# Kernel tuning notes

Hardware: AMD Instinct MI355X
Metric: run time of the kernel (lower is better)

## Reference

```python
import jax, jax.numpy as jnp
import numpy as np
from jax import lax

NPOINT = 1024
NSAMPLE = 64
RADIUS = 0.2
EPS = 1e-5  # BatchNorm eps


def farthest_point_sample(xyz, npoint):
    # xyz: [B, N, 3] -> idx [B, npoint]; deterministic init at point 0
    B, N, _ = xyz.shape

    def step(carry, _):
        dist, farthest = carry
        centroid = jnp.take_along_axis(xyz, farthest[:, None, None], axis=1)  # [B,1,3]
        d = jnp.sum((xyz - centroid) ** 2, axis=-1)  # [B,N]
        dist = jnp.minimum(dist, d)
        new_far = jnp.argmax(dist, axis=-1).astype(jnp.int32)
        return (dist, new_far), farthest

    init = (jnp.full((B, N), 1e10, xyz.dtype), jnp.zeros((B,), jnp.int32))
    _, idxs = lax.scan(step, init, None, length=npoint)
    return jnp.transpose(idxs)  # [B, npoint]


def square_distance(src, dst):
    # src [B,S,3], dst [B,N,3] -> [B,S,N]
    d = -2.0 * jnp.einsum('bsc,bnc->bsn', src, dst)
    d += jnp.sum(src ** 2, -1)[:, :, None]
    d += jnp.sum(dst ** 2, -1)[:, None, :]
    return d


def query_ball_point(radius, nsample, xyz, new_xyz):
    B, N, _ = xyz.shape
    sqr = square_distance(new_xyz, xyz)  # [B,S,N]
    gi = jnp.where(sqr > radius ** 2, N, jnp.arange(N, dtype=jnp.int32))
    gi = jnp.sort(gi, axis=-1)[:, :, :nsample]  # [B,S,K]
    first = gi[:, :, :1]
    gi = jnp.where(gi == N, first, gi)
    return gi


def mlp_bn_relu(x, W, g, b):
    # x [B,S,K,Cin], W [Cin,Cout]; 1x1 conv + training-mode BN + ReLU
    y = jnp.einsum('bskc,co->bsko', x, W)
    m = jnp.mean(y, axis=(0, 1, 2))
    v = jnp.var(y, axis=(0, 1, 2))
    y = (y - m) * lax.rsqrt(v + EPS) * g + b
    return jax.nn.relu(y)


def setup_inputs() -> dict:
    key = jax.random.key(0)
    ks = jax.random.split(key, 8)
    B, N, C = 8, 4096, 128
    xyz = jax.random.uniform(ks[0], (B, N, 3), dtype=jnp.float32)
    features = jax.random.normal(ks[1], (B, C, N), dtype=jnp.float32)
    c_in = C + 3  # use_xyz
    W1 = jax.random.normal(ks[2], (c_in, 128), dtype=jnp.float32) * 0.05
    W2 = jax.random.normal(ks[3], (128, 128), dtype=jnp.float32) * 0.05
    W3 = jax.random.normal(ks[4], (128, 256), dtype=jnp.float32) * 0.05
    return {
        'xyz': xyz, 'features': features,
        'W1': W1, 'g1': jnp.ones((128,)), 'b1': jnp.zeros((128,)),
        'W2': W2, 'g2': jnp.ones((128,)), 'b2': jnp.zeros((128,)),
        'W3': W3, 'g3': jnp.ones((256,)), 'b3': jnp.zeros((256,)),
    }


def reference(xyz, features, W1, g1, b1, W2, g2, b2, W3, g3, b3):
    fps_idx = farthest_point_sample(xyz, NPOINT)              # [B,S]
    new_xyz = jnp.take_along_axis(xyz, fps_idx[:, :, None], axis=1)  # [B,S,3]
    gi = query_ball_point(RADIUS, NSAMPLE, xyz, new_xyz)      # [B,S,K]
    gather = jax.vmap(lambda p, i: p[i])                      # per-batch gather
    grouped_xyz = gather(xyz, gi) - new_xyz[:, :, None, :]    # [B,S,K,3]
    grouped_feat = gather(jnp.transpose(features, (0, 2, 1)), gi)  # [B,S,K,C]
    x = jnp.concatenate([grouped_xyz, grouped_feat], axis=-1)  # [B,S,K,3+C]
    x = mlp_bn_relu(x, W1, g1, b1)
    x = mlp_bn_relu(x, W2, g2, b2)
    x = mlp_bn_relu(x, W3, g3, b3)
    new_features = jnp.transpose(jnp.max(x, axis=2), (0, 2, 1))  # [B,256,S]
    return new_xyz, new_features
```

## Files before the change

### kernel.cpp

```cpp
#include <hip/hip_runtime.h>

#define B_  8
#define N_  4096
#define S_  1024
#define K_  64
#define CF_ 128
#define M_  (B_*S_*K_)

typedef __attribute__((ext_vector_type(8))) short bshort8;
typedef __attribute__((ext_vector_type(4))) float f32x4;
typedef __attribute__((ext_vector_type(4))) int   i32x4;
typedef __attribute__((ext_vector_type(2))) float f32x2;
typedef __attribute__((ext_vector_type(4))) unsigned short us4;

__device__ __forceinline__ unsigned short f2bf(float f){
  unsigned int u = __float_as_uint(f);
  u = u + 0x7FFFu + ((u >> 16) & 1u);
  return (unsigned short)(u >> 16);
}
__device__ __forceinline__ float bf2f(unsigned short h){
  return __uint_as_float(((unsigned int)h) << 16);
}

#define DPP_PAIR_STEP(CTRL)                                                     \
  {                                                                             \
    int _vi = __builtin_amdgcn_update_dpp(__float_as_int(best), __float_as_int(best), (CTRL), 0xF, 0xF, false); \
    int _ii = __builtin_amdgcn_update_dpp(bidx, bidx, (CTRL), 0xF, 0xF, false); \
    float _ov = __int_as_float(_vi);                                            \
    bool _tk = (_ov > best) || (_ov == best && _ii < bidx);                     \
    best = _tk ? _ov : best;                                                    \
    bidx = _tk ? _ii : bidx;                                                    \
  }

__global__ __launch_bounds__(256) void fps_kernel(const float* __restrict__ xyz,
                                                  float* __restrict__ nx_out,
                                                  float* __restrict__ nx_ws){
#pragma clang fp contract(off)
  __shared__ float sx[N_], sy[N_], sz[N_];
  __shared__ int   sidx[S_];
  __shared__ alignas(16) float redv[2][4];
  __shared__ alignas(16) int   redi[2][4];
  const int b = blockIdx.x, t = threadIdx.x;
  const int lane = t & 63, w = t >> 6;
  const float* xb = xyz + (size_t)b*N_*3;
  f32x2 px[8], py[8], pz[8], dist[8];
#pragma unroll
  for (int j=0;j<8;++j){
    int i0 = (2*j)*256 + t, i1 = (2*j+1)*256 + t;
    float x0=xb[i0*3+0], y0=xb[i0*3+1], z0=xb[i0*3+2];
    float x1=xb[i1*3+0], y1=xb[i1*3+1], z1=xb[i1*3+2];
    px[j] = (f32x2){x0,x1}; py[j] = (f32x2){y0,y1}; pz[j] = (f32x2){z0,z1};
    dist[j] = (f32x2){1e10f,1e10f};
    sx[i0]=x0; sy[i0]=y0; sz[i0]=z0;
    sx[i1]=x1; sy[i1]=y1; sz[i1]=z1;
  }
  __syncthreads();
  int farthest = 0;
  for (int it=0; it<S_; ++it){
    if (t==0) sidx[it] = farthest;
    float cx = sx[farthest], cy = sy[farthest], cz = sz[farthest];
    f32x2 cx2 = (f32x2){cx,cx}, cy2 = (f32x2){cy,cy}, cz2 = (f32x2){cz,cz};
    float best = -1.0f; int bidx = 0;
#pragma unroll
    for (int j=0;j<8;++j){
      f32x2 dx = px[j] - cx2;
      f32x2 dy = py[j] - cy2;
      f32x2 dz = pz[j] - cz2;
      f32x2 d  = (dx*dx + dy*dy) + dz*dz;
      f32x2 nd;
      nd.x = fminf(dist[j].x, d.x);
      nd.y = fminf(dist[j].y, d.y);
      dist[j] = nd;
      bool tk0 = nd.x > best;
      best = tk0 ? nd.x : best;
      bidx = tk0 ? ((2*j)*256 + t) : bidx;
      bool tk1 = nd.y > best;
      best = tk1 ? nd.y : best;
      bidx = tk1 ? ((2*j+1)*256 + t) : bidx;
    }
    DPP_PAIR_STEP(0xB1);
    DPP_PAIR_STEP(0x4E);
    DPP_PAIR_STEP(0x124);
    DPP_PAIR_STEP(0x128);
    DPP_PAIR_STEP(0x142);
    DPP_PAIR_STEP(0x143);
    const int buf = it & 1;
    if (lane == 63){ redv[buf][w] = best; redi[buf][w] = bidx; }
    __syncthreads();
    f32x4 vv = *(const f32x4*)&redv[buf][0];
    i32x4 iv = *(const i32x4*)&redi[buf][0];
    float v01 = vv[0]; int i01 = iv[0];
    { bool tk = (vv[1] > v01) || (vv[1] == v01 && iv[1] < i01); v01 = tk?vv[1]:v01; i01 = tk?iv[1]:i01; }
    float v23 = vv[2]; int i23 = iv[2];
    { bool tk = (vv[3] > v23) || (vv[3] == v23 && iv[3] < i23); v23 = tk?vv[3]:v23; i23 = tk?iv[3]:i23; }
    { bool tk = (v23 > v01) || (v23 == v01 && i23 < i01); v01 = tk?v23:v01; i01 = tk?i23:i01; }
    farthest = i01;
  }
  __syncthreads();
  for (int i=t; i<S_; i+=256){
    int id = sidx[i];
    size_t base = (size_t)(b*S_+i)*3;
    float vx=sx[id], vy=sy[id], vz=sz[id];
    nx_out[base+0]=vx; nx_out[base+1]=vy; nx_out[base+2]=vz;
    nx_ws[base+0]=vx;  nx_ws[base+1]=vy;  nx_ws[base+2]=vz;
  }
}

__global__ __launch_bounds__(256) void qbp_kernel(const float* __restrict__ xyz,
                                                  const float* __restrict__ nx,
                                                  int* __restrict__ gi){
  const double R2 = 0.2*0.2;
  int gtid = blockIdx.x*256 + threadIdx.x;
  int wid = gtid >> 6, lane = gtid & 63;
  int b = wid >> 10, s = wid & 1023;
  const float* xb = xyz + (size_t)b*N_*3;
  const float* c  = nx + (size_t)(b*S_+s)*3;
  double cx=(double)c[0], cy=(double)c[1], cz=(double)c[2];
  double cc = cx*cx + cy*cy + cz*cz;
  int* g = gi + (size_t)(b*S_+s)*K_;
  int count = 0, first = -1;
  for (int ch=0; ch<64 && count<K_; ++ch){
    int i = ch*64 + lane;
    double x = (double)xb[i*3+0], y = (double)xb[i*3+1], z = (double)xb[i*3+2];
    double e  = cx*x + cy*y + cz*z;
    double pp = x*x + y*y + z*z;
    double d  = -2.0*e + cc + pp;
    bool keep = !(d > R2);
    unsigned long long bal = __ballot(keep);
    int pos = count + __builtin_popcountll(bal & ((1ull<<lane)-1ull));
    if (keep && pos < K_) g[pos] = i;
    if (first < 0 && bal) first = ch*64 + (int)__builtin_ctzll(bal);
    count += __builtin_popcountll(bal);
  }
  if (count < K_){
    int p = count + lane;
    if (p < K_) g[p] = first;
  }
}

__global__ __launch_bounds__(256) void transpose_kernel(const float* __restrict__ f,
                                                        unsigned short* __restrict__ ft){
  __shared__ float tile[32][33];
  int b = blockIdx.z, ct = blockIdx.y, nt = blockIdx.x;
  int tx = threadIdx.x & 31, ty = threadIdx.x >> 5;
#pragma unroll
  for (int r=0; r<32; r+=8)
    tile[ty+r][tx] = f[((size_t)(b*128 + ct*32 + ty + r))*4096 + nt*32 + tx];
  __syncthreads();
#pragma unroll
  for (int r=0; r<32; r+=8){
    int n = nt*32 + ty + r, cc = ct*32 + tx;
    ft[((size_t)b*4096 + n)*128 + cc] = f2bf(tile[tx][ty+r]);
  }
}

__global__ void wprep_kernel(const float* __restrict__ W1, const float* __restrict__ W2,
                             const float* __restrict__ W3,
                             unsigned short* __restrict__ Wt1, unsigned short* __restrict__ Wt2,
                             unsigned short* __restrict__ Wt3){
  int t = blockIdx.x*blockDim.x + threadIdx.x;
  int stride = gridDim.x*blockDim.x;
  for (int idx=t; idx<128*160; idx+=stride){
    int n = idx/160, k = idx-(idx/160)*160;
    float v = 0.f;
    if (k < 128) v = W1[(k+3)*128 + n];
    else if (k < 131) v = W1[(k-128)*128 + n];
    Wt1[idx] = f2bf(v);
  }
  for (int idx=t; idx<128*128; idx+=stride){
    int n = idx>>7, k = idx&127;
    Wt2[idx] = f2bf(W2[k*128+n]);
  }
  for (int idx=t; idx<256*128; idx+=stride){
    int n = idx>>7, k = idx&127;
    Wt3[idx] = f2bf(W3[k*256+n]);
  }
}

__global__ __launch_bounds__(256,2) void pgemm_kernel(const unsigned short* __restrict__ featT,
                                                      const unsigned short* __restrict__ Wt1,
                                                      float* __restrict__ P){
  __shared__ alignas(16) unsigned short At[128*40];
  __shared__ alignas(16) unsigned short Bt[128*40];
  const int t = threadIdx.x, blk = blockIdx.x;
  const size_t rowBase = (size_t)blk*128;
  const int lane = t&63, wave = t>>6;
  const int wm = wave>>1, wn = wave&1;
  const int lrow = lane&15, quad = lane>>4;
  f32x4 acc[4][4];
  const f32x4 z4 = {0.f,0.f,0.f,0.f};
#pragma unroll
  for (int i=0;i<4;++i)
#pragma unroll
    for (int j=0;j<4;++j) acc[i][j]=z4;
  for (int ch=0; ch<4; ++ch){
    __syncthreads();
#pragma unroll
    for (int half=0; half<2; ++half){
      int sl = t + half*256; int r = sl>>2, p = sl&3;
      *(bshort8*)&At[r*40+p*8] = *(const bshort8*)(featT + (rowBase + r)*CF_ + ch*32 + p*8);
      *(bshort8*)&Bt[r*40+p*8] = *(const bshort8*)(Wt1 + r*160 + ch*32 + p*8);
    }
    __syncthreads();
    bshort8 af[4], bfr[4];
#pragma unroll
    for (int mt=0; mt<4; ++mt) af[mt]  = *(const bshort8*)&At[(wm*64+mt*16+lrow)*40 + quad*8];
#pragma unroll
    for (int nt=0; nt<4; ++nt) bfr[nt] = *(const bshort8*)&Bt[(wn*64+nt*16+lrow)*40 + quad*8];
#pragma unroll
    for (int mt=0; mt<4; ++mt)
#pragma unroll
      for (int nt=0; nt<4; ++nt)
        acc[mt][nt] = __builtin_amdgcn_mfma_f32_16x16x32_bf16(af[mt], bfr[nt], acc[mt][nt], 0,0,0);
  }
#pragma unroll
  for (int mt=0; mt<4; ++mt)
#pragma unroll
    for (int nt=0; nt<4; ++nt)
#pragma unroll
      for (int r=0; r<4; ++r){
        int row = wm*64 + mt*16 + quad*4 + r;
        int col = wn*64 + nt*16 + lrow;
        P[(rowBase + row)*128 + col] = acc[mt][nt][r];
      }
}

template<int PHASE>
__global__ __launch_bounds__(256,2) void mm_fused(
    const float* __restrict__ P,
    const float* __restrict__ W1,
    const unsigned short* __restrict__ Wt2,
    const unsigned short* __restrict__ Wt3,
    const int* __restrict__ gi,
    const float* __restrict__ xyz,
    const float* __restrict__ nxyz,
    const float* __restrict__ ss1,
    const float* __restrict__ ss2,
    float* __restrict__ slots,
    float* __restrict__ minv,
    float* __restrict__ maxv)
{
  __shared__ alignas(16) unsigned short Bt[2][(PHASE>=2)?(128*40):8];
  __shared__ alignas(16) unsigned short Y[(PHASE>=2)?(128*136):16];
  __shared__ int giL[128];
  __shared__ alignas(16) float dxL[128][4];
  __shared__ alignas(16) float w0L[128], w1L[128], w2L[128];
  __shared__ float sLDS[(PHASE==1)?128:4], s2LDS[(PHASE==1)?128:4];

  const int t = threadIdx.x;
  const int mblk = blockIdx.x;
  const int b = mblk >> 9;
  const int lane = t&63, wave = t>>6;
  const int wm = wave>>1, wn = wave&1;
  const int lrow = lane&15, quad = lane>>4;
  const int slot = mblk & 63;

  if (t<128){
    int i = gi[(size_t)mblk*128 + t];
    giL[t] = i;
    int s = ((mblk*128 + t) >> 6) & 1023;
    const float* pp = xyz  + ((size_t)b*N_ + i)*3;
    const float* qq = nxyz + (size_t)(b*S_ + s)*3;
    dxL[t][0] = __fsub_rn(pp[0],qq[0]);
    dxL[t][1] = __fsub_rn(pp[1],qq[1]);
    dxL[t][2] = __fsub_rn(pp[2],qq[2]);
    w0L[t] = W1[t]; w1L[t] = W1[128+t]; w2L[t] = W1[256+t];
    if constexpr (PHASE==1){ sLDS[t]=0.f; s2LDS[t]=0.f; }
  }
  __syncthreads();

  {
    const int rgrp = t>>5, cq = (t&31)*4;
    f32x4 w0 = *(const f32x4*)&w0L[cq];
    f32x4 w1 = *(const f32x4*)&w1L[cq];
    f32x4 w2 = *(const f32x4*)&w2L[cq];
    f32x4 a1v, b1v;
    if constexpr (PHASE>=2){
      a1v = *(const f32x4*)(ss1 + cq);
      b1v = *(const f32x4*)(ss1 + 128 + cq);
    }
    f32x4 sA = {0,0,0,0}, s2A = {0,0,0,0};
#pragma unroll
    for (int g=0; g<16; ++g){
      int r = g*8 + rgrp;
      int pi = giL[r];
      f32x4 p = *(const f32x4*)(P + ((size_t)b*N_ + pi)*128 + cq);
      float dx = dxL[r][0], dy = dxL[r][1], dz = dxL[r][2];
      f32x4 y;
#pragma unroll
      for (int e=0;e<4;++e)
        y[e] = fmaf(dz, w2[e], fmaf(dy, w1[e], fmaf(dx, w0[e], p[e])));
      if constexpr (PHASE==1){
#pragma unroll
        for (int e=0;e<4;++e){ sA[e] += y[e]; s2A[e] = fmaf(y[e], y[e], s2A[e]); }
      } else {
        us4 zz;
#pragma unroll
        for (int e=0;e<4;++e)
          zz[e] = f2bf(fmaxf(fmaf(y[e], a1v[e], b1v[e]), 0.f));
        *(us4*)&Y[r*136 + cq] = zz;
      }
    }
    if constexpr (PHASE==1){
#pragma unroll
      for (int e=0;e<4;++e){
        atomicAdd(&sLDS[cq+e],  sA[e]);
        atomicAdd(&s2LDS[cq+e], s2A[e]);
      }
      __syncthreads();
      if (t<128){
        atomicAdd(&slots[(slot*128+t)*2+0], sLDS[t]);
        atomicAdd(&slots[(slot*128+t)*2+1], s2LDS[t]);
      }
      return;
    }
  }

  if constexpr (PHASE>=2){
    f32x4 acc[4][4];
    const f32x4 z4 = {0.f,0.f,0.f,0.f};
#pragma unroll
    for (int i=0;i<4;++i)
#pragma unroll
      for (int j=0;j<4;++j) acc[i][j]=z4;

    {
      bshort8 bV[2];
#pragma unroll
      for (int half=0; half<2; ++half){
        int sl = t + half*256; int r = sl>>2, p = sl&3;
        bV[half] = *(const bshort8*)(Wt2 + r*128 + p*8);
      }
#pragma unroll
      for (int half=0; half<2; ++half){
        int sl = t + half*256; int r = sl>>2, p = sl&3;
        *(bshort8*)&Bt[1][r*40+p*8] = bV[half];
      }
      for (int ch=0; ch<4; ++ch){
        const int cur = (ch & 1) ^ 1;
        __syncthreads();
        bshort8 af[4], bfr[4];
#pragma unroll
        for (int mt=0; mt<4; ++mt) af[mt]  = *(const bshort8*)&Y[(wm*64+mt*16+lrow)*136 + ch*32 + quad*8];
#pragma unroll
        for (int nt=0; nt<4; ++nt) bfr[nt] = *(const bshort8*)&Bt[cur][(wn*64+nt*16+lrow)*40 + quad*8];
        if (ch < 3){
#pragma unroll
          for (int half=0; half<2; ++half){
            int sl = t + half*256; int r = sl>>2, p = sl&3;
            bV[half] = *(const bshort8*)(Wt2 + r*128 + (ch+1)*32 + p*8);
          }
        }
#pragma unroll
        for (int mt=0; mt<4; ++mt)
#pragma unroll
          for (int nt=0; nt<4; ++nt)
            acc[mt][nt] = __builtin_amdgcn_mfma_f32_16x16x32_bf16(af[mt], bfr[nt], acc[mt][nt], 0,0,0);
        if (ch < 3){
          const int nxt = cur ^ 1;
#pragma unroll
          for (int half=0; half<2; ++half){
            int sl = t + half*256; int r = sl>>2, p = sl&3;
            *(bshort8*)&Bt[nxt][r*40+p*8] = bV[half];
          }
        }
      }
    }

    if constexpr (PHASE==2){
#pragma unroll
      for (int nt=0; nt<4; ++nt){
        float s=0.f, s2=0.f;
#pragma unroll
        for (int mt=0; mt<4; ++mt)
#pragma unroll
          for (int r=0; r<4; ++r){ float v=acc[mt][nt][r]; s+=v; s2=fmaf(v,v,s2); }
        s  += __shfl_xor(s,16,64);  s  += __shfl_xor(s,32,64);
        s2 += __shfl_xor(s2,16,64); s2 += __shfl_xor(s2,32,64);
        if (lane<16){
          int c = wn*64+nt*16+lane;
          atomicAdd(&slots[(slot*128+c)*2+0], s);
          atomicAdd(&slots[(slot*128+c)*2+1], s2);
        }
      }
      return;
    }

    if constexpr (PHASE==3){
      __syncthreads();
#pragma unroll
      for (int nt=0; nt<4; ++nt){
        int c = wn*64+nt*16+lrow;
        float sc = ss2[c], sh = ss2[128+c];
#pragma unroll
        for (int mt=0; mt<4; ++mt)
#pragma unroll
          for (int r=0; r<4; ++r){
            int row = wm*64+mt*16+quad*4+r;
            Y[row*136 + c] = f2bf(fmaxf(fmaf(acc[mt][nt][r], sc, sh), 0.f));
          }
      }

      for (int h=0; h<2; ++h){
#pragma unroll
        for (int i=0;i<4;++i)
#pragma unroll
          for (int j=0;j<4;++j) acc[i][j]=z4;
        bshort8 bV[2];
#pragma unroll
        for (int half=0; half<2; ++half){
          int sl = t + half*256; int r = sl>>2, p = sl&3;
          bV[half] = *(const bshort8*)(Wt3 + ((size_t)(h*128+r))*128 + p*8);
        }
#pragma unroll
        for (int half=0; half<2; ++half){
          int sl = t + half*256; int r = sl>>2, p = sl&3;
          *(bshort8*)&Bt[1][r*40+p*8] = bV[half];
        }
        for (int ch=0; ch<4; ++ch){
          const int cur = (ch & 1) ^ 1;
          __syncthreads();
          bshort8 af[4], bfr[4];
#pragma unroll
          for (int mt=0; mt<4; ++mt) af[mt]  = *(const bshort8*)&Y[(wm*64+mt*16+lrow)*136 + ch*32 + quad*8];
#pragma unroll
          for (int nt=0; nt<4; ++nt) bfr[nt] = *(const bshort8*)&Bt[cur][(wn*64+nt*16+lrow)*40 + quad*8];
          if (ch < 3){
#pragma unroll
            for (int half=0; half<2; ++half){
              int sl = t + half*256; int r = sl>>2, p = sl&3;
              bV[half] = *(const bshort8*)(Wt3 + ((size_t)(h*128+r))*128 + (ch+1)*32 + p*8);
            }
          }
#pragma unroll
          for (int mt=0; mt<4; ++mt)
#pragma unroll
            for (int nt=0; nt<4; ++nt)
              acc[mt][nt] = __builtin_amdgcn_mfma_f32_16x16x32_bf16(af[mt], bfr[nt], acc[mt][nt], 0,0,0);
          if (ch < 3){
            const int nxt = cur ^ 1;
#pragma unroll
            for (int half=0; half<2; ++half){
              int sl = t + half*256; int r = sl>>2, p = sl&3;
              *(bshort8*)&Bt[nxt][r*40+p*8] = bV[half];
            }
          }
        }
#pragma unroll
        for (int nt=0; nt<4; ++nt){
          float s=0.f, s2=0.f, mx=-3.0e38f, mn=3.0e38f;
#pragma unroll
          for (int mt=0; mt<4; ++mt)
#pragma unroll
            for (int r=0; r<4; ++r){
              float v=acc[mt][nt][r];
              s+=v; s2=fmaf(v,v,s2);
              mx=fmaxf(mx,v); mn=fminf(mn,v);
            }
          s  += __shfl_xor(s,16,64);  s  += __shfl_xor(s,32,64);
          s2 += __shfl_xor(s2,16,64); s2 += __shfl_xor(s2,32,64);
          mx = fmaxf(mx, __shfl_xor(mx,16,64)); mx = fmaxf(mx, __shfl_xor(mx,32,64));
          mn = fminf(mn, __shfl_xor(mn,16,64)); mn = fminf(mn, __shfl_xor(mn,32,64));
          if (lane<16){
            int c = h*128 + wn*64+nt*16+lane;
            atomicAdd(&slots[(slot*256+c)*2+0], s);
            atomicAdd(&slots[(slot*256+c)*2+1], s2);
            size_t sidx = (size_t)mblk*2 + wm;
            maxv[sidx*256 + c] = mx;
            minv[sidx*256 + c] = mn;
          }
        }
      }
    }
  }
}

__global__ void stats_kernel(const float* __restrict__ slots, const float* __restrict__ g,
                             const float* __restrict__ beta, float* __restrict__ ssOut,
                             int C, float inv_cnt){
  int c = threadIdx.x;
  if (c >= C) return;
  float s=0.f, s2=0.f;
  for (int k=0;k<64;++k){
    s  += slots[(k*C + c)*2 + 0];
    s2 += slots[(k*C + c)*2 + 1];
  }
  float m = s * inv_cnt;
  float v = fmaxf(s2 * inv_cnt - m*m, 0.f);
  float sc = rsqrtf(v + 1e-5f) * g[c];
  ssOut[c] = sc;
  ssOut[C + c] = beta[c] - m*sc;
}

__global__ __launch_bounds__(256) void final_kernel(const float* __restrict__ minv,
                                                    const float* __restrict__ maxv,
                                                    const float* __restrict__ ss3,
                                                    float* __restrict__ out){
  __shared__ float tile[64][65];
  const int t = threadIdx.x;
  const int cb = blockIdx.x;
  const int sb = blockIdx.y;
  const int b  = blockIdx.z;
  const int w = t>>6, l = t&63;
  {
    int c = cb*64 + l;
    float sc = ss3[c], sh = ss3[256+c];
#pragma unroll
    for (int k=0;k<16;++k){
      int sl = k*4 + w;
      size_t mi = ((size_t)(b*1024 + sb*64 + sl))*256 + c;
      float v = (sc >= 0.f) ? maxv[mi] : minv[mi];
      tile[sl][l] = fmaxf(fmaf(v, sc, sh), 0.f);
    }
  }
  __syncthreads();
#pragma unroll
  for (int k=0;k<16;++k){
    int cl = k*4 + w;
    out[((size_t)(b*256 + cb*64 + cl))*1024 + sb*64 + l] = tile[l][cl];
  }
}

extern "C" void kernel_launch(void* const* d_in, const int* in_sizes, int n_in,
                              void* d_out, int out_size, void* d_ws, size_t ws_size,
                              hipStream_t stream){
  const float* xyz      = (const float*)d_in[0];
  const float* features = (const float*)d_in[1];
  const float* W1 = (const float*)d_in[2];
  const float* g1 = (const float*)d_in[3];
  const float* b1 = (const float*)d_in[4];
  const float* W2 = (const float*)d_in[5];
  const float* g2 = (const float*)d_in[6];
  const float* b2 = (const float*)d_in[7];
  const float* W3 = (const float*)d_in[8];
  const float* g3 = (const float*)d_in[9];
  const float* b3 = (const float*)d_in[10];
  float* out = (float*)d_out;

  char* ws = (char*)d_ws;
  size_t off = 0;
  auto alloc = [&](size_t bytes)->char*{
    char* p = ws + off;
    off = (off + bytes + 255) & ~(size_t)255;
    return p;
  };
  float* slots1 = (float*)alloc((size_t)64*128*2*4);
  float* slots2 = (float*)alloc((size_t)64*128*2*4);
  float* slots3 = (float*)alloc((size_t)64*256*2*4);
  float* ss1    = (float*)alloc(256*4);
  float* ss2    = (float*)alloc(256*4);
  float* ss3    = (float*)alloc(512*4);
  float* nxyz   = (float*)alloc((size_t)24576*4);
  int*   gi     = (int*)  alloc((size_t)M_*4);
  unsigned short* featT = (unsigned short*)alloc((size_t)B_*N_*CF_*2);
  unsigned short* Wt1   = (unsigned short*)alloc((size_t)128*160*2);
  unsigned short* Wt2   = (unsigned short*)alloc((size_t)128*128*2);
  unsigned short* Wt3   = (unsigned short*)alloc((size_t)256*128*2);
  float* minv = (float*)alloc((size_t)B_*S_*256*4);
  float* maxv = (float*)alloc((size_t)B_*S_*256*4);
  float* P    = (float*)alloc((size_t)B_*N_*128*4);

  hipMemsetAsync(slots1, 0, (size_t)(64*128*2 + 64*128*2 + 64*256*2)*4, stream);

  transpose_kernel<<<dim3(128,4,8), 256, 0, stream>>>(features, featT);
  wprep_kernel<<<64, 256, 0, stream>>>(W1, W2, W3, Wt1, Wt2, Wt3);
  pgemm_kernel<<<256, 256, 0, stream>>>(featT, Wt1, P);
  fps_kernel<<<8, 256, 0, stream>>>(xyz, out, nxyz);
  qbp_kernel<<<2048, 256, 0, stream>>>(xyz, nxyz, gi);

  const float inv_cnt = 1.0f / (float)M_;
  mm_fused<1><<<4096, 256, 0, stream>>>(P, W1, Wt2, Wt3, gi, xyz, nxyz,
                                        nullptr, nullptr, slots1, nullptr, nullptr);
  stats_kernel<<<1, 128, 0, stream>>>(slots1, g1, b1, ss1, 128, inv_cnt);
  mm_fused<2><<<4096, 256, 0, stream>>>(P, W1, Wt2, Wt3, gi, xyz, nxyz,
                                        ss1, nullptr, slots2, nullptr, nullptr);
  stats_kernel<<<1, 128, 0, stream>>>(slots2, g2, b2, ss2, 128, inv_cnt);
  mm_fused<3><<<4096, 256, 0, stream>>>(P, W1, Wt2, Wt3, gi, xyz, nxyz,
                                        ss1, ss2, slots3, minv, maxv);
  stats_kernel<<<1, 256, 0, stream>>>(slots3, g3, b3, ss3, 256, inv_cnt);
  final_kernel<<<dim3(4,16,8), 256, 0, stream>>>(minv, maxv, ss3, out + 24576);
}
```

Measured before the change: 1.144 ms.

## Merge prep kernels, co-schedule FPS with feature GEMM, fuse ball query with layer-1 stats

The transpose and weight-prep kernels are merged into one launch. The serial 8-block FPS kernel now shares a launch with the 256-block feature GEMM, so the GEMM blocks run on otherwise idle CUs while FPS iterates. The ball query is fused with the layer-1 statistics pass, which removes the separate mm_fused<1> launch and the re-read of gi. The tradeoffs are a larger shared-memory footprint for the combined kernel and one wave per centroid doing the stats loop.

```diff
diff --git a/kernel.cpp b/kernel.cpp
--- a/kernel.cpp
+++ b/kernel.cpp
@@ -20,6 +20,49 @@
 }
 __device__ __forceinline__ float bf2f(unsigned short h){
   return __uint_as_float(((unsigned int)h) << 16);
+}
+
+__global__ __launch_bounds__(256) void prep_kernel(const float* __restrict__ f,
+                                                   const float* __restrict__ W1,
+                                                   const float* __restrict__ W2,
+                                                   const float* __restrict__ W3,
+                                                   unsigned short* __restrict__ ft,
+                                                   unsigned short* __restrict__ Wt1,
+                                                   unsigned short* __restrict__ Wt2,
+                                                   unsigned short* __restrict__ Wt3){
+  __shared__ float tile[32][33];
+  const int blk = blockIdx.x;
+  if (blk < 4096){
+    int nt = blk & 127, ct = (blk>>7)&3, b = blk>>9;
+    int tx = threadIdx.x & 31, ty = threadIdx.x >> 5;
+#pragma unroll
+    for (int r=0; r<32; r+=8)
+      tile[ty+r][tx] = f[((size_t)(b*128 + ct*32 + ty + r))*4096 + nt*32 + tx];
+    __syncthreads();
+#pragma unroll
+    for (int r=0; r<32; r+=8){
+      int n = nt*32 + ty + r, cc = ct*32 + tx;
+      ft[((size_t)b*4096 + n)*128 + cc] = f2bf(tile[tx][ty+r]);
+    }
+  } else {
+    int t = (blk-4096)*256 + threadIdx.x;
+    int stride = 64*256;
+    for (int idx=t; idx<128*160; idx+=stride){
+      int n = idx/160, k = idx-(idx/160)*160;
+      float v = 0.f;
+      if (k < 128) v = W1[(k+3)*128 + n];
+      else if (k < 131) v = W1[(k-128)*128 + n];
+      Wt1[idx] = f2bf(v);
+    }
+    for (int idx=t; idx<128*128; idx+=stride){
+      int n = idx>>7, k = idx&127;
+      Wt2[idx] = f2bf(W2[k*128+n]);
+    }
+    for (int idx=t; idx<256*128; idx+=stride){
+      int n = idx>>7, k = idx&127;
+      Wt3[idx] = f2bf(W3[k*256+n]);
+    }
+  }
 }
 
 #define DPP_PAIR_STEP(CTRL)                                                     \
@@ -32,197 +75,207 @@
     bidx = _tk ? _ii : bidx;                                                    \
   }
 
-__global__ __launch_bounds__(256) void fps_kernel(const float* __restrict__ xyz,
-                                                  float* __restrict__ nx_out,
-                                                  float* __restrict__ nx_ws){
+__global__ __launch_bounds__(256) void fps_pgemm_kernel(const float* __restrict__ xyz,
+                                                        float* __restrict__ nx_out,
+                                                        float* __restrict__ nx_ws,
+                                                        const unsigned short* __restrict__ featT,
+                                                        const unsigned short* __restrict__ Wt1,
+                                                        float* __restrict__ P){
 #pragma clang fp contract(off)
-  __shared__ float sx[N_], sy[N_], sz[N_];
-  __shared__ int   sidx[S_];
-  __shared__ alignas(16) float redv[2][4];
-  __shared__ alignas(16) int   redi[2][4];
-  const int b = blockIdx.x, t = threadIdx.x;
+  __shared__ alignas(16) char smem[53312];
+  const int t = threadIdx.x;
+  if (blockIdx.x < 8){
+    float* sx = (float*)smem;
+    float* sy = (float*)(smem+16384);
+    float* sz = (float*)(smem+32768);
+    int*   sidx = (int*)(smem+49152);
+    float (*redv)[4] = (float(*)[4])(smem+53248);
+    int   (*redi)[4] = (int(*)[4])(smem+53280);
+    const int b = blockIdx.x;
+    const int lane = t & 63, w = t >> 6;
+    const float* xb = xyz + (size_t)b*N_*3;
+    f32x2 px[8], py[8], pz[8], dist[8];
+#pragma unroll
+    for (int j=0;j<8;++j){
+      int i0 = (2*j)*256 + t, i1 = (2*j+1)*256 + t;
+      float x0=xb[i0*3+0], y0=xb[i0*3+1], z0=xb[i0*3+2];
+      float x1=xb[i1*3+0], y1=xb[i1*3+1], z1=xb[i1*3+2];
+      px[j] = (f32x2){x0,x1}; py[j] = (f32x2){y0,y1}; pz[j] = (f32x2){z0,z1};
+      dist[j] = (f32x2){1e10f,1e10f};
+      sx[i0]=x0; sy[i0]=y0; sz[i0]=z0;
+      sx[i1]=x1; sy[i1]=y1; sz[i1]=z1;
+    }
+    __syncthreads();
+    int farthest = 0;
+    for (int it=0; it<S_; ++it){
+      if (t==0) sidx[it] = farthest;
+      float cx = sx[farthest], cy = sy[farthest], cz = sz[farthest];
+      f32x2 cx2 = (f32x2){cx,cx}, cy2 = (f32x2){cy,cy}, cz2 = (f32x2){cz,cz};
+      float best = -1.0f; int bidx = 0;
+#pragma unroll
+      for (int j=0;j<8;++j){
+        f32x2 dx = px[j] - cx2;
+        f32x2 dy = py[j] - cy2;
+        f32x2 dz = pz[j] - cz2;
+        f32x2 d  = (dx*dx + dy*dy) + dz*dz;
+        f32x2 nd;
+        nd.x = fminf(dist[j].x, d.x);
+        nd.y = fminf(dist[j].y, d.y);
+        dist[j] = nd;
+        bool tk0 = nd.x > best;
+        best = tk0 ? nd.x : best;
+        bidx = tk0 ? ((2*j)*256 + t) : bidx;
+        bool tk1 = nd.y > best;
+        best = tk1 ? nd.y : best;
+        bidx = tk1 ? ((2*j+1)*256 + t) : bidx;
+      }
+      DPP_PAIR_STEP(0xB1);
+      DPP_PAIR_STEP(0x4E);
+      DPP_PAIR_STEP(0x124);
+      DPP_PAIR_STEP(0x128);
+      DPP_PAIR_STEP(0x142);
+      DPP_PAIR_STEP(0x143);
+      const int buf = it & 1;
+      if (lane == 63){ redv[buf][w] = best; redi[buf][w] = bidx; }
+      __syncthreads();
+      f32x4 vv = *(const f32x4*)&redv[buf][0];
+      i32x4 iv = *(const i32x4*)&redi[buf][0];
+      float v01 = vv[0]; int i01 = iv[0];
+      { bool tk = (vv[1] > v01) || (vv[1] == v01 && iv[1] < i01); v01 = tk?vv[1]:v01; i01 = tk?iv[1]:i01; }
+      float v23 = vv[2]; int i23 = iv[2];
+      { bool tk = (vv[3] > v23) || (vv[3] == v23 && iv[3] < i23); v23 = tk?vv[3]:v23; i23 = tk?iv[3]:i23; }
+      { bool tk = (v23 > v01) || (v23 == v01 && i23 < i01); v01 = tk?v23:v01; i01 = tk?i23:i01; }
+      farthest = i01;
+    }
+    __syncthreads();
+    for (int i=t; i<S_; i+=256){
+      int id = sidx[i];
+      size_t base = (size_t)(b*S_+i)*3;
+      float vx=sx[id], vy=sy[id], vz=sz[id];
+      nx_out[base+0]=vx; nx_out[base+1]=vy; nx_out[base+2]=vz;
+      nx_ws[base+0]=vx;  nx_ws[base+1]=vy;  nx_ws[base+2]=vz;
+    }
+  } else {
+    unsigned short* At = (unsigned short*)smem;
+    unsigned short* Bt = (unsigned short*)(smem+10240);
+    const int blk = blockIdx.x - 8;
+    const size_t rowBase = (size_t)blk*128;
+    const int lane = t&63, wave = t>>6;
+    const int wm = wave>>1, wn = wave&1;
+    const int lrow = lane&15, quad = lane>>4;
+    f32x4 acc[4][4];
+    const f32x4 z4 = {0.f,0.f,0.f,0.f};
+#pragma unroll
+    for (int i=0;i<4;++i)
+#pragma unroll
+      for (int j=0;j<4;++j) acc[i][j]=z4;
+    for (int ch=0; ch<4; ++ch){
+      __syncthreads();
+#pragma unroll
+      for (int half=0; half<2; ++half){
+        int sl = t + half*256; int r = sl>>2, p = sl&3;
+        *(bshort8*)&At[r*40+p*8] = *(const bshort8*)(featT + (rowBase + r)*CF_ + ch*32 + p*8);
+        *(bshort8*)&Bt[r*40+p*8] = *(const bshort8*)(Wt1 + r*160 + ch*32 + p*8);
+      }
+      __syncthreads();
+      bshort8 af[4], bfr[4];
+#pragma unroll
+      for (int mt=0; mt<4; ++mt) af[mt]  = *(const bshort8*)&At[(wm*64+mt*16+lrow)*40 + quad*8];
+#pragma unroll
+      for (int nt=0; nt<4; ++nt) bfr[nt] = *(const bshort8*)&Bt[(wn*64+nt*16+lrow)*40 + quad*8];
+#pragma unroll
+      for (int mt=0; mt<4; ++mt)
+#pragma unroll
+        for (int nt=0; nt<4; ++nt)
+          acc[mt][nt] = __builtin_amdgcn_mfma_f32_16x16x32_bf16(af[mt], bfr[nt], acc[mt][nt], 0,0,0);
+    }
+#pragma unroll
+    for (int mt=0; mt<4; ++mt)
+#pragma unroll
+      for (int nt=0; nt<4; ++nt)
+#pragma unroll
+        for (int r=0; r<4; ++r){
+          int row = wm*64 + mt*16 + quad*4 + r;
+          int col = wn*64 + nt*16 + lrow;
+          P[(rowBase + row)*128 + col] = acc[mt][nt][r];
+        }
+  }
+}
+
+__global__ __launch_bounds__(256) void qbp_y1_kernel(const float* __restrict__ xyz,
+                                                     const float* __restrict__ nx,
+                                                     const float* __restrict__ P,
+                                                     const float* __restrict__ W1,
+                                                     int* __restrict__ gi,
+                                                     float* __restrict__ slots){
+  __shared__ int giW[4][64];
+  __shared__ alignas(16) float dxL[4][64][4];
+  __shared__ float sLDS[128], s2LDS[128];
+  const int t = threadIdx.x;
   const int lane = t & 63, w = t >> 6;
+  if (t < 128){ sLDS[t]=0.f; s2LDS[t]=0.f; }
+  __syncthreads();
+  const int wid = blockIdx.x*4 + w;
+  const int b = wid >> 10, s = wid & 1023;
   const float* xb = xyz + (size_t)b*N_*3;
-  f32x2 px[8], py[8], pz[8], dist[8];
-#pragma unroll
-  for (int j=0;j<8;++j){
-    int i0 = (2*j)*256 + t, i1 = (2*j+1)*256 + t;
-    float x0=xb[i0*3+0], y0=xb[i0*3+1], z0=xb[i0*3+2];
-    float x1=xb[i1*3+0], y1=xb[i1*3+1], z1=xb[i1*3+2];
-    px[j] = (f32x2){x0,x1}; py[j] = (f32x2){y0,y1}; pz[j] = (f32x2){z0,z1};
-    dist[j] = (f32x2){1e10f,1e10f};
-    sx[i0]=x0; sy[i0]=y0; sz[i0]=z0;
-    sx[i1]=x1; sy[i1]=y1; sz[i1]=z1;
+  {
+    const double R2 = 0.2*0.2;
+    const float* c  = nx + (size_t)(b*S_+s)*3;
+    double cx=(double)c[0], cy=(double)c[1], cz=(double)c[2];
+    double cc = cx*cx + cy*cy + cz*cz;
+    int* g = gi + (size_t)(b*S_+s)*K_;
+    int count = 0, first = -1;
+    for (int ch=0; ch<64 && count<K_; ++ch){
+      int i = ch*64 + lane;
+      double x = (double)xb[i*3+0], y = (double)xb[i*3+1], z = (double)xb[i*3+2];
+      double e  = cx*x + cy*y + cz*z;
+      double pp = x*x + y*y + z*z;
+      double d  = -2.0*e + cc + pp;
+      bool keep = !(d > R2);
+      unsigned long long bal = __ballot(keep);
+      int pos = count + __builtin_popcountll(bal & ((1ull<<lane)-1ull));
+      if (keep && pos < K_){ g[pos] = i; giW[w][pos] = i; }
+      if (first < 0 && bal) first = ch*64 + (int)__builtin_ctzll(bal);
+      count += __builtin_popcountll(bal);
+    }
+    if (count < K_){
+      int p = count + lane;
+      if (p < K_){ g[p] = first; giW[w][p] = first; }
+    }
+    int i = giW[w][lane];
+    const float* pp = xyz + ((size_t)b*N_ + i)*3;
+    const float* qq = nx  + (size_t)(b*S_ + s)*3;
+    dxL[w][lane][0] = __fsub_rn(pp[0],qq[0]);
+    dxL[w][lane][1] = __fsub_rn(pp[1],qq[1]);
+    dxL[w][lane][2] = __fsub_rn(pp[2],qq[2]);
+  }
+  {
+    const int cq = lane*2;
+    f32x2 w0 = *(const f32x2*)(W1 + cq);
+    f32x2 w1v = *(const f32x2*)(W1 + 128 + cq);
+    f32x2 w2 = *(const f32x2*)(W1 + 256 + cq);
+    f32x2 sA = {0,0}, s2A = {0,0};
+#pragma unroll 4
+    for (int r=0; r<64; ++r){
+      int pi = giW[w][r];
+      f32x2 p = *(const f32x2*)(P + ((size_t)b*N_ + pi)*128 + cq);
+      float dx = dxL[w][r][0], dy = dxL[w][r][1], dz = dxL[w][r][2];
+      f32x2 y;
+#pragma unroll
+      for (int e=0;e<2;++e)
+        y[e] = fmaf(dz, w2[e], fmaf(dy, w1v[e], fmaf(dx, w0[e], p[e])));
+      sA.x += y.x; sA.y += y.y;
+      s2A.x = fmaf(y.x,y.x,s2A.x); s2A.y = fmaf(y.y,y.y,s2A.y);
+    }
+    atomicAdd(&sLDS[cq],    sA.x);  atomicAdd(&sLDS[cq+1],  sA.y);
+    atomicAdd(&s2LDS[cq],   s2A.x); atomicAdd(&s2LDS[cq+1], s2A.y);
   }
   __syncthreads();
-  int farthest = 0;
-  for (int it=0; it<S_; ++it){
-    if (t==0) sidx[it] = farthest;
-    float cx = sx[farthest], cy = sy[farthest], cz = sz[farthest];
-    f32x2 cx2 = (f32x2){cx,cx}, cy2 = (f32x2){cy,cy}, cz2 = (f32x2){cz,cz};
-    float best = -1.0f; int bidx = 0;
-#pragma unroll
-    for (int j=0;j<8;++j){
-      f32x2 dx = px[j] - cx2;
-      f32x2 dy = py[j] - cy2;
-      f32x2 dz = pz[j] - cz2;
-      f32x2 d  = (dx*dx + dy*dy) + dz*dz;
-      f32x2 nd;
-      nd.x = fminf(dist[j].x, d.x);
-      nd.y = fminf(dist[j].y, d.y);
-      dist[j] = nd;
-      bool tk0 = nd.x > best;
-      best = tk0 ? nd.x : best;
-      bidx = tk0 ? ((2*j)*256 + t) : bidx;
-      bool tk1 = nd.y > best;
-      best = tk1 ? nd.y : best;
-      bidx = tk1 ? ((2*j+1)*256 + t) : bidx;
-    }
-    DPP_PAIR_STEP(0xB1);
-    DPP_PAIR_STEP(0x4E);
-    DPP_PAIR_STEP(0x124);
-    DPP_PAIR_STEP(0x128);
-    DPP_PAIR_STEP(0x142);
-    DPP_PAIR_STEP(0x143);
-    const int buf = it & 1;
-    if (lane == 63){ redv[buf][w] = best; redi[buf][w] = bidx; }
-    __syncthreads();
-    f32x4 vv = *(const f32x4*)&redv[buf][0];
-    i32x4 iv = *(const i32x4*)&redi[buf][0];
-    float v01 = vv[0]; int i01 = iv[0];
-    { bool tk = (vv[1] > v01) || (vv[1] == v01 && iv[1] < i01); v01 = tk?vv[1]:v01; i01 = tk?iv[1]:i01; }
-    float v23 = vv[2]; int i23 = iv[2];
-    { bool tk = (vv[3] > v23) || (vv[3] == v23 && iv[3] < i23); v23 = tk?vv[3]:v23; i23 = tk?iv[3]:i23; }
-    { bool tk = (v23 > v01) || (v23 == v01 && i23 < i01); v01 = tk?v23:v01; i01 = tk?i23:i01; }
-    farthest = i01;
-  }
-  __syncthreads();
-  for (int i=t; i<S_; i+=256){
-    int id = sidx[i];
-    size_t base = (size_t)(b*S_+i)*3;
-    float vx=sx[id], vy=sy[id], vz=sz[id];
-    nx_out[base+0]=vx; nx_out[base+1]=vy; nx_out[base+2]=vz;
-    nx_ws[base+0]=vx;  nx_ws[base+1]=vy;  nx_ws[base+2]=vz;
-  }
-}
-
-__global__ __launch_bounds__(256) void qbp_kernel(const float* __restrict__ xyz,
-                                                  const float* __restrict__ nx,
-                                                  int* __restrict__ gi){
-  const double R2 = 0.2*0.2;
-  int gtid = blockIdx.x*256 + threadIdx.x;
-  int wid = gtid >> 6, lane = gtid & 63;
-  int b = wid >> 10, s = wid & 1023;
-  const float* xb = xyz + (size_t)b*N_*3;
-  const float* c  = nx + (size_t)(b*S_+s)*3;
-  double cx=(double)c[0], cy=(double)c[1], cz=(double)c[2];
-  double cc = cx*cx + cy*cy + cz*cz;
-  int* g = gi + (size_t)(b*S_+s)*K_;
-  int count = 0, first = -1;
-  for (int ch=0; ch<64 && count<K_; ++ch){
-    int i = ch*64 + lane;
-    double x = (double)xb[i*3+0], y = (double)xb[i*3+1], z = (double)xb[i*3+2];
-    double e  = cx*x + cy*y + cz*z;
-    double pp = x*x + y*y + z*z;
-    double d  = -2.0*e + cc + pp;
-    bool keep = !(d > R2);
-    unsigned long long bal = __ballot(keep);
-    int pos = count + __builtin_popcountll(bal & ((1ull<<lane)-1ull));
-    if (keep && pos < K_) g[pos] = i;
-    if (first < 0 && bal) first = ch*64 + (int)__builtin_ctzll(bal);
-    count += __builtin_popcountll(bal);
-  }
-  if (count < K_){
-    int p = count + lane;
-    if (p < K_) g[p] = first;
-  }
-}
-
-__global__ __launch_bounds__(256) void transpose_kernel(const float* __restrict__ f,
-                                                        unsigned short* __restrict__ ft){
-  __shared__ float tile[32][33];
-  int b = blockIdx.z, ct = blockIdx.y, nt = blockIdx.x;
-  int tx = threadIdx.x & 31, ty = threadIdx.x >> 5;
-#pragma unroll
-  for (int r=0; r<32; r+=8)
-    tile[ty+r][tx] = f[((size_t)(b*128 + ct*32 + ty + r))*4096 + nt*32 + tx];
-  __syncthreads();
-#pragma unroll
-  for (int r=0; r<32; r+=8){
-    int n = nt*32 + ty + r, cc = ct*32 + tx;
-    ft[((size_t)b*4096 + n)*128 + cc] = f2bf(tile[tx][ty+r]);
-  }
-}
-
-__global__ void wprep_kernel(const float* __restrict__ W1, const float* __restrict__ W2,
-                             const float* __restrict__ W3,
-                             unsigned short* __restrict__ Wt1, unsigned short* __restrict__ Wt2,
-                             unsigned short* __restrict__ Wt3){
-  int t = blockIdx.x*blockDim.x + threadIdx.x;
-  int stride = gridDim.x*blockDim.x;
-  for (int idx=t; idx<128*160; idx+=stride){
-    int n = idx/160, k = idx-(idx/160)*160;
-    float v = 0.f;
-    if (k < 128) v = W1[(k+3)*128 + n];
-    else if (k < 131) v = W1[(k-128)*128 + n];
-    Wt1[idx] = f2bf(v);
-  }
-  for (int idx=t; idx<128*128; idx+=stride){
-    int n = idx>>7, k = idx&127;
-    Wt2[idx] = f2bf(W2[k*128+n]);
-  }
-  for (int idx=t; idx<256*128; idx+=stride){
-    int n = idx>>7, k = idx&127;
-    Wt3[idx] = f2bf(W3[k*256+n]);
-  }
-}
-
-__global__ __launch_bounds__(256,2) void pgemm_kernel(const unsigned short* __restrict__ featT,
-                                                      const unsigned short* __restrict__ Wt1,
-                                                      float* __restrict__ P){
-  __shared__ alignas(16) unsigned short At[128*40];
-  __shared__ alignas(16) unsigned short Bt[128*40];
-  const int t = threadIdx.x, blk = blockIdx.x;
-  const size_t rowBase = (size_t)blk*128;
-  const int lane = t&63, wave = t>>6;
-  const int wm = wave>>1, wn = wave&1;
-  const int lrow = lane&15, quad = lane>>4;
-  f32x4 acc[4][4];
-  const f32x4 z4 = {0.f,0.f,0.f,0.f};
-#pragma unroll
-  for (int i=0;i<4;++i)
-#pragma unroll
-    for (int j=0;j<4;++j) acc[i][j]=z4;
-  for (int ch=0; ch<4; ++ch){
-    __syncthreads();
-#pragma unroll
-    for (int half=0; half<2; ++half){
-      int sl = t + half*256; int r = sl>>2, p = sl&3;
-      *(bshort8*)&At[r*40+p*8] = *(const bshort8*)(featT + (rowBase + r)*CF_ + ch*32 + p*8);
-      *(bshort8*)&Bt[r*40+p*8] = *(const bshort8*)(Wt1 + r*160 + ch*32 + p*8);
-    }
-    __syncthreads();
-    bshort8 af[4], bfr[4];
-#pragma unroll
-    for (int mt=0; mt<4; ++mt) af[mt]  = *(const bshort8*)&At[(wm*64+mt*16+lrow)*40 + quad*8];
-#pragma unroll
-    for (int nt=0; nt<4; ++nt) bfr[nt] = *(const bshort8*)&Bt[(wn*64+nt*16+lrow)*40 + quad*8];
-#pragma unroll
-    for (int mt=0; mt<4; ++mt)
-#pragma unroll
-      for (int nt=0; nt<4; ++nt)
-        acc[mt][nt] = __builtin_amdgcn_mfma_f32_16x16x32_bf16(af[mt], bfr[nt], acc[mt][nt], 0,0,0);
-  }
-#pragma unroll
-  for (int mt=0; mt<4; ++mt)
-#pragma unroll
-    for (int nt=0; nt<4; ++nt)
-#pragma unroll
-      for (int r=0; r<4; ++r){
-        int row = wm*64 + mt*16 + quad*4 + r;
-        int col = wn*64 + nt*16 + lrow;
-        P[(rowBase + row)*128 + col] = acc[mt][nt][r];
-      }
+  if (t < 128){
+    int slot = blockIdx.x & 63;
+    atomicAdd(&slots[(slot*128+t)*2+0], sLDS[t]);
+    atomicAdd(&slots[(slot*128+t)*2+1], s2LDS[t]);
+  }
 }
 
 template<int PHASE>
@@ -240,12 +293,11 @@
     float* __restrict__ minv,
     float* __restrict__ maxv)
 {
-  __shared__ alignas(16) unsigned short Bt[2][(PHASE>=2)?(128*40):8];
-  __shared__ alignas(16) unsigned short Y[(PHASE>=2)?(128*136):16];
+  __shared__ alignas(16) unsigned short Bt[2][128*40];
+  __shared__ alignas(16) unsigned short Y[128*136];
   __shared__ int giL[128];
   __shared__ alignas(16) float dxL[128][4];
   __shared__ alignas(16) float w0L[128], w1L[128], w2L[128];
-  __shared__ float sLDS[(PHASE==1)?128:4], s2LDS[(PHASE==1)?128:4];
 
   const int t = threadIdx.x;
   const int mblk = blockIdx.x;
@@ -265,7 +317,6 @@
     dxL[t][1] = __fsub_rn(pp[1],qq[1]);
     dxL[t][2] = __fsub_rn(pp[2],qq[2]);
     w0L[t] = W1[t]; w1L[t] = W1[128+t]; w2L[t] = W1[256+t];
-    if constexpr (PHASE==1){ sLDS[t]=0.f; s2LDS[t]=0.f; }
   }
   __syncthreads();
 
@@ -274,12 +325,8 @@
     f32x4 w0 = *(const f32x4*)&w0L[cq];
     f32x4 w1 = *(const f32x4*)&w1L[cq];
     f32x4 w2 = *(const f32x4*)&w2L[cq];
-    f32x4 a1v, b1v;
-    if constexpr (PHASE>=2){
-      a1v = *(const f32x4*)(ss1 + cq);
-      b1v = *(const f32x4*)(ss1 + 128 + cq);
-    }
-    f32x4 sA = {0,0,0,0}, s2A = {0,0,0,0};
+    f32x4 a1v = *(const f32x4*)(ss1 + cq);
+    f32x4 b1v = *(const f32x4*)(ss1 + 128 + cq);
 #pragma unroll
     for (int g=0; g<16; ++g){
       int r = g*8 + rgrp;
@@ -290,46 +337,108 @@
 #pragma unroll
       for (int e=0;e<4;++e)
         y[e] = fmaf(dz, w2[e], fmaf(dy, w1[e], fmaf(dx, w0[e], p[e])));
-      if constexpr (PHASE==1){
-#pragma unroll
-        for (int e=0;e<4;++e){ sA[e] += y[e]; s2A[e] = fmaf(y[e], y[e], s2A[e]); }
-      } else {
-        us4 zz;
-#pragma unroll
-        for (int e=0;e<4;++e)
-          zz[e] = f2bf(fmaxf(fmaf(y[e], a1v[e], b1v[e]), 0.f));
-        *(us4*)&Y[r*136 + cq] = zz;
-      }
-    }
-    if constexpr (PHASE==1){
-#pragma unroll
-      for (int e=0;e<4;++e){
-        atomicAdd(&sLDS[cq+e],  sA[e]);
-        atomicAdd(&s2LDS[cq+e], s2A[e]);
-      }
+      us4 zz;
+#pragma unroll
+      for (int e=0;e<4;++e)
+        zz[e] = f2bf(fmaxf(fmaf(y[e], a1v[e], b1v[e]), 0.f));
+      *(us4*)&Y[r*136 + cq] = zz;
+    }
+  }
+
+  f32x4 acc[4][4];
+  const f32x4 z4 = {0.f,0.f,0.f,0.f};
+#pragma unroll
+  for (int i=0;i<4;++i)
+#pragma unroll
+    for (int j=0;j<4;++j) acc[i][j]=z4;
+
+  {
+    bshort8 bV[2];
+#pragma unroll
+    for (int half=0; half<2; ++half){
+      int sl = t + half*256; int r = sl>>2, p = sl&3;
+      bV[half] = *(const bshort8*)(Wt2 + r*128 + p*8);
+    }
+#pragma unroll
+    for (int half=0; half<2; ++half){
+      int sl = t + half*256; int r = sl>>2, p = sl&3;
+      *(bshort8*)&Bt[1][r*40+p*8] = bV[half];
+    }
+    for (int ch=0; ch<4; ++ch){
+      const int cur = (ch & 1) ^ 1;
       __syncthreads();
-      if (t<128){
-        atomicAdd(&slots[(slot*128+t)*2+0], sLDS[t]);
-        atomicAdd(&slots[(slot*128+t)*2+1], s2LDS[t]);
-      }
-      return;
-    }
-  }
-
-  if constexpr (PHASE>=2){
-    f32x4 acc[4][4];
-    const f32x4 z4 = {0.f,0.f,0.f,0.f};
-#pragma unroll
-    for (int i=0;i<4;++i)
-#pragma unroll
-      for (int j=0;j<4;++j) acc[i][j]=z4;
-
-    {
+      bshort8 af[4], bfr[4];
+#pragma unroll
+      for (int mt=0; mt<4; ++mt) af[mt]  = *(const bshort8*)&Y[(wm*64+mt*16+lrow)*136 + ch*32 + quad*8];
+#pragma unroll
+      for (int nt=0; nt<4; ++nt) bfr[nt] = *(const bshort8*)&Bt[cur][(wn*64+nt*16+lrow)*40 + quad*8];
+      if (ch < 3){
+#pragma unroll
+        for (int half=0; half<2; ++half){
+          int sl = t + half*256; int r = sl>>2, p = sl&3;
+          bV[half] = *(const bshort8*)(Wt2 + r*128 + (ch+1)*32 + p*8);
+        }
+      }
+#pragma unroll
+      for (int mt=0; mt<4; ++mt)
+#pragma unroll
+        for (int nt=0; nt<4; ++nt)
+          acc[mt][nt] = __builtin_amdgcn_mfma_f32_16x16x32_bf16(af[mt], bfr[nt], acc[mt][nt], 0,0,0);
+      if (ch < 3){
+        const int nxt = cur ^ 1;
+#pragma unroll
+        for (int half=0; half<2; ++half){
+          int sl = t + half*256; int r = sl>>2, p = sl&3;
+          *(bshort8*)&Bt[nxt][r*40+p*8] = bV[half];
+        }
+      }
+    }
+  }
+
+  if constexpr (PHASE==2){
+#pragma unroll
+    for (int nt=0; nt<4; ++nt){
+      float s=0.f, s2=0.f;
+#pragma unroll
+      for (int mt=0; mt<4; ++mt)
+#pragma unroll
+        for (int r=0; r<4; ++r){ float v=acc[mt][nt][r]; s+=v; s2=fmaf(v,v,s2); }
+      s  += __shfl_xor(s,16,64);  s  += __shfl_xor(s,32,64);
+      s2 += __shfl_xor(s2,16,64); s2 += __shfl_xor(s2,32,64);
+      if (lane<16){
+        int c = wn*64+nt*16+lane;
+        atomicAdd(&slots[(slot*128+c)*2+0], s);
+        atomicAdd(&slots[(slot*128+c)*2+1], s2);
+      }
+    }
+    return;
+  }
+
+  if constexpr (PHASE==3){
+    __syncthreads();
+#pragma unroll
+    for (int nt=0; nt<4; ++nt){
+      int c = wn*64+nt*16+lrow;
+      float sc = ss2[c], sh = ss2[128+c];
+#pragma unroll
+      for (int mt=0; mt<4; ++mt)
+#pragma unroll
+        for (int r=0; r<4; ++r){
+          int row = wm*64+mt*16+quad*4+r;
+          Y[row*136 + c] = f2bf(fmaxf(fmaf(acc[mt][nt][r], sc, sh), 0.f));
+        }
+    }
+
+    for (int h=0; h<2; ++h){
+#pragma unroll
+      for (int i=0;i<4;++i)
+#pragma unroll
+        for (int j=0;j<4;++j) acc[i][j]=z4;
       bshort8 bV[2];
 #pragma unroll
       for (int half=0; half<2; ++half){
         int sl = t + half*256; int r = sl>>2, p = sl&3;
-        bV[half] = *(const bshort8*)(Wt2 + r*128 + p*8);
+        bV[half] = *(const bshort8*)(Wt3 + ((size_t)(h*128+r))*128 + p*8);
       }
 #pragma unroll
       for (int half=0; half<2; ++half){
@@ -348,7 +457,7 @@
 #pragma unroll
           for (int half=0; half<2; ++half){
             int sl = t + half*256; int r = sl>>2, p = sl&3;
-            bV[half] = *(const bshort8*)(Wt2 + r*128 + (ch+1)*32 + p*8);
+            bV[half] = *(const bshort8*)(Wt3 + ((size_t)(h*128+r))*128 + (ch+1)*32 + p*8);
           }
         }
 #pragma unroll
@@ -365,110 +474,28 @@
           }
         }
       }
-    }
-
-    if constexpr (PHASE==2){
 #pragma unroll
       for (int nt=0; nt<4; ++nt){
-        float s=0.f, s2=0.f;
+        float s=0.f, s2=0.f, mx=-3.0e38f, mn=3.0e38f;
 #pragma unroll
         for (int mt=0; mt<4; ++mt)
 #pragma unroll
-          for (int r=0; r<4; ++r){ float v=acc[mt][nt][r]; s+=v; s2=fmaf(v,v,s2); }
+          for (int r=0; r<4; ++r){
+            float v=acc[mt][nt][r];
+            s+=v; s2=fmaf(v,v,s2);
+            mx=fmaxf(mx,v); mn=fminf(mn,v);
+          }
         s  += __shfl_xor(s,16,64);  s  += __shfl_xor(s,32,64);
         s2 += __shfl_xor(s2,16,64); s2 += __shfl_xor(s2,32,64);
+        mx = fmaxf(mx, __shfl_xor(mx,16,64)); mx = fmaxf(mx, __shfl_xor(mx,32,64));
+        mn = fminf(mn, __shfl_xor(mn,16,64)); mn = fminf(mn, __shfl_xor(mn,32,64));
         if (lane<16){
-          int c = wn*64+nt*16+lane;
-          atomicAdd(&slots[(slot*128+c)*2+0], s);
-          atomicAdd(&slots[(slot*128+c)*2+1], s2);
-        }
-      }
-      return;
-    }
-
-    if constexpr (PHASE==3){
-      __syncthreads();
-#pragma unroll
-      for (int nt=0; nt<4; ++nt){
-        int c = wn*64+nt*16+lrow;
-        float sc = ss2[c], sh = ss2[128+c];
-#pragma unroll
-        for (int mt=0; mt<4; ++mt)
-#pragma unroll
-          for (int r=0; r<4; ++r){
-            int row = wm*64+mt*16+quad*4+r;
-            Y[row*136 + c] = f2bf(fmaxf(fmaf(acc[mt][nt][r], sc, sh), 0.f));
-          }
-      }
-
-      for (int h=0; h<2; ++h){
-#pragma unroll
-        for (int i=0;i<4;++i)
-#pragma unroll
-          for (int j=0;j<4;++j) acc[i][j]=z4;
-        bshort8 bV[2];
-#pragma unroll
-        for (int half=0; half<2; ++half){
-          int sl = t + half*256; int r = sl>>2, p = sl&3;
-          bV[half] = *(const bshort8*)(Wt3 + ((size_t)(h*128+r))*128 + p*8);
-        }
-#pragma unroll
-        for (int half=0; half<2; ++half){
-          int sl = t + half*256; int r = sl>>2, p = sl&3;
-          *(bshort8*)&Bt[1][r*40+p*8] = bV[half];
-        }
-        for (int ch=0; ch<4; ++ch){
-          const int cur = (ch & 1) ^ 1;
-          __syncthreads();
-          bshort8 af[4], bfr[4];
-#pragma unroll
-          for (int mt=0; mt<4; ++mt) af[mt]  = *(const bshort8*)&Y[(wm*64+mt*16+lrow)*136 + ch*32 + quad*8];
-#pragma unroll
-          for (int nt=0; nt<4; ++nt) bfr[nt] = *(const bshort8*)&Bt[cur][(wn*64+nt*16+lrow)*40 + quad*8];
-          if (ch < 3){
-#pragma unroll
-            for (int half=0; half<2; ++half){
-              int sl = t + half*256; int r = sl>>2, p = sl&3;
-              bV[half] = *(const bshort8*)(Wt3 + ((size_t)(h*128+r))*128 + (ch+1)*32 + p*8);
-            }
-          }
-#pragma unroll
-          for (int mt=0; mt<4; ++mt)
-#pragma unroll
-            for (int nt=0; nt<4; ++nt)
-              acc[mt][nt] = __builtin_amdgcn_mfma_f32_16x16x32_bf16(af[mt], bfr[nt], acc[mt][nt], 0,0,0);
-          if (ch < 3){
-            const int nxt = cur ^ 1;
-#pragma unroll
-            for (int half=0; half<2; ++half){
-              int sl = t + half*256; int r = sl>>2, p = sl&3;
-              *(bshort8*)&Bt[nxt][r*40+p*8] = bV[half];
-            }
-          }
-        }
-#pragma unroll
-        for (int nt=0; nt<4; ++nt){
-          float s=0.f, s2=0.f, mx=-3.0e38f, mn=3.0e38f;
-#pragma unroll
-          for (int mt=0; mt<4; ++mt)
-#pragma unroll
-            for (int r=0; r<4; ++r){
-              float v=acc[mt][nt][r];
-              s+=v; s2=fmaf(v,v,s2);
-              mx=fmaxf(mx,v); mn=fminf(mn,v);
-            }
-          s  += __shfl_xor(s,16,64);  s  += __shfl_xor(s,32,64);
-          s2 += __shfl_xor(s2,16,64); s2 += __shfl_xor(s2,32,64);
-          mx = fmaxf(mx, __shfl_xor(mx,16,64)); mx = fmaxf(mx, __shfl_xor(mx,32,64));
-          mn = fminf(mn, __shfl_xor(mn,16,64)); mn = fminf(mn, __shfl_xor(mn,32,64));
-          if (lane<16){
-            int c = h*128 + wn*64+nt*16+lane;
-            atomicAdd(&slots[(slot*256+c)*2+0], s);
-            atomicAdd(&slots[(slot*256+c)*2+1], s2);
-            size_t sidx = (size_t)mblk*2 + wm;
-            maxv[sidx*256 + c] = mx;
-            minv[sidx*256 + c] = mn;
-          }
+          int c = h*128 + wn*64+nt*16+lane;
+          atomicAdd(&slots[(slot*256+c)*2+0], s);
+          atomicAdd(&slots[(slot*256+c)*2+1], s2);
+          size_t sidx = (size_t)mblk*2 + wm;
+          maxv[sidx*256 + c] = mx;
+          minv[sidx*256 + c] = mn;
         }
       }
     }
@@ -562,15 +589,11 @@
 
   hipMemsetAsync(slots1, 0, (size_t)(64*128*2 + 64*128*2 + 64*256*2)*4, stream);
 
-  transpose_kernel<<<dim3(128,4,8), 256, 0, stream>>>(features, featT);
-  wprep_kernel<<<64, 256, 0, stream>>>(W1, W2, W3, Wt1, Wt2, Wt3);
-  pgemm_kernel<<<256, 256, 0, stream>>>(featT, Wt1, P);
-  fps_kernel<<<8, 256, 0, stream>>>(xyz, out, nxyz);
-  qbp_kernel<<<2048, 256, 0, stream>>>(xyz, nxyz, gi);
+  prep_kernel<<<4160, 256, 0, stream>>>(features, W1, W2, W3, featT, Wt1, Wt2, Wt3);
+  fps_pgemm_kernel<<<264, 256, 0, stream>>>(xyz, out, nxyz, featT, Wt1, P);
+  qbp_y1_kernel<<<2048, 256, 0, stream>>>(xyz, nxyz, P, W1, gi, slots1);
 
   const float inv_cnt = 1.0f / (float)M_;
-  mm_fused<1><<<4096, 256, 0, stream>>>(P, W1, Wt2, Wt3, gi, xyz, nxyz,
-                                        nullptr, nullptr, slots1, nullptr, nullptr);
   stats_kernel<<<1, 128, 0, stream>>>(slots1, g1, b1, ss1, 128, inv_cnt);
   mm_fused<2><<<4096, 256, 0, stream>>>(P, W1, Wt2, Wt3, gi, xyz, nxyz,
                                         ss1, nullptr, slots2, nullptr, nullptr);
```

After: 1.127 ms. About the same (-1.6%).
